# Performance work log

Hardware: AMD Instinct MI355X
Metric: run time of the kernel (lower is better)

## Reference

```python
import jax, jax.numpy as jnp
import numpy as np

B, T, D, H, O, E, K = 2, 2048, 1024, 4096, 1024, 8, 2


def setup_inputs() -> dict:
    key = jax.random.key(0)
    ks = jax.random.split(key, 10)
    s = 0.02  # small init scale to keep activations well-conditioned
    return {
        "x": jax.random.normal(ks[0], (B, T, D), jnp.float32),
        "noise": jax.random.normal(ks[1], (B, T, E), jnp.float32),
        "Wg": jax.random.normal(ks[2], (D, E), jnp.float32) * s,
        "bg": jnp.zeros((E,), jnp.float32),
        "Wn": jax.random.normal(ks[3], (D, E), jnp.float32) * s,
        "bn": jnp.zeros((E,), jnp.float32),
        "W1": jax.random.normal(ks[4], (E, D, H), jnp.float32) * s,
        "b1": jnp.zeros((E, H), jnp.float32),
        "W2": jax.random.normal(ks[5], (E, H, O), jnp.float32) * s,
        "b2": jnp.zeros((E, O), jnp.float32),
    }


def reference(x, noise, Wg, bg, Wn, bn, W1, b1, W2, b2):
    # --- NoisyTopkRouter ---
    logits = x @ Wg + bg                    # [B,T,E]
    noise_logits = x @ Wn + bn              # [B,T,E]
    noisy = logits + noise * jax.nn.softplus(noise_logits)
    top_v, top_i = jax.lax.top_k(noisy, K)  # [B,T,K]
    # scatter top-k logits into a -inf background, softmax -> sparse gates
    mask = jax.nn.one_hot(top_i, E, dtype=noisy.dtype).sum(-2)  # [B,T,E] in {0,1}
    sparse_logits = jnp.where(mask > 0, noisy, -jnp.inf)
    gating = jax.nn.softmax(sparse_logits, axis=-1)
    # mask + L1 normalize (F.normalize p=1, dim=2)
    gating = gating * mask
    gating = gating / jnp.maximum(jnp.sum(jnp.abs(gating), axis=-1, keepdims=True), 1e-12)
    # --- dense run of ALL experts (faithful to the naive torch module) ---
    h = jax.nn.relu(jnp.einsum('btd,edh->beth', x, W1) + b1[:, None, :])   # [B,E,T,H]
    expert_out = jnp.einsum('beth,eho->beto', h, W2) + b2[:, None, :]       # [B,E,T,O]
    # combine: torch transposes to [B,T,E,O] then einsum 'bte,bteo->bto'
    out = jnp.einsum('bte,beto->bto', gating, expert_out)                   # [B,T,O]
    return out
```

## Files before the change

kernel.cpp:

```cpp
#include <hip/hip_runtime.h>
#include <hip/hip_bf16.h>

#define TOK 4096
#define DD  1024
#define HH  4096
#define OO  1024
#define EE  8

#define TPE        16
#define SLOT_STRUCT (EE * TPE)
#define SLOT_OVF   64
#define SLOT_TOTAL (SLOT_STRUCT + SLOT_OVF)
#define MAX_ACTIVE 72

typedef float  f32x4  __attribute__((ext_vector_type(4)));
typedef __bf16 bf16x8 __attribute__((ext_vector_type(8)));
typedef __bf16 bf16x4 __attribute__((ext_vector_type(4)));
typedef unsigned int u32x4 __attribute__((ext_vector_type(4)));

union ABCast { u32x4 u; bf16x8 b; };

typedef __attribute__((address_space(3))) unsigned int       lds_uint;
typedef const __attribute__((address_space(1))) unsigned int glob_uint;

__device__ __forceinline__ void gload_lds16(void* lds, const void* g) {
    __builtin_amdgcn_global_load_lds((glob_uint*)g, (lds_uint*)lds, 16, 0, 0);
}

__global__ void router_kernel(const float* __restrict__ x, const float* __restrict__ noise,
                              const float* __restrict__ Wg, const float* __restrict__ bg,
                              const float* __restrict__ Wn, const float* __restrict__ bn,
                              int* __restrict__ topk_e, float* __restrict__ topk_g,
                              int* __restrict__ cnt)
{
    int wave = threadIdx.x >> 6;
    int lane = threadIdx.x & 63;
    int token = blockIdx.x * 4 + wave;
    const float* xr = x + (size_t)token * DD;
    float accg[EE], accn[EE];
#pragma unroll
    for (int e = 0; e < EE; ++e) { accg[e] = 0.f; accn[e] = 0.f; }
    for (int jj = 0; jj < DD / 64; ++jj) {
        int d = lane + jj * 64;
        float xv = xr[d];
        const float* wgr = Wg + d * EE;
        const float* wnr = Wn + d * EE;
#pragma unroll
        for (int e = 0; e < EE; ++e) {
            accg[e] += xv * wgr[e];
            accn[e] += xv * wnr[e];
        }
    }
#pragma unroll
    for (int off = 32; off; off >>= 1) {
#pragma unroll
        for (int e = 0; e < EE; ++e) {
            accg[e] += __shfl_down(accg[e], off, 64);
            accn[e] += __shfl_down(accn[e], off, 64);
        }
    }
    if (lane == 0) {
        float noisy[EE];
#pragma unroll
        for (int e = 0; e < EE; ++e) {
            float lg = accg[e] + bg[e];
            float nl = accn[e] + bn[e];
            float sp = fmaxf(nl, 0.f) + log1pf(expf(-fabsf(nl)));
            noisy[e] = lg + noise[(size_t)token * EE + e] * sp;
        }
        int i1 = 0; float v1 = noisy[0];
#pragma unroll
        for (int e = 1; e < EE; ++e) if (noisy[e] > v1) { v1 = noisy[e]; i1 = e; }
        int i2 = -1; float v2 = -1e30f;
#pragma unroll
        for (int e = 0; e < EE; ++e) if (e != i1 && noisy[e] > v2) { v2 = noisy[e]; i2 = e; }
        float ex = expf(v2 - v1);
        float g1 = 1.f / (1.f + ex);
        float g2 = ex / (1.f + ex);
        topk_e[token * 2] = i1;  topk_e[token * 2 + 1] = i2;
        topk_g[token * 2] = g1;  topk_g[token * 2 + 1] = g2;
        atomicAdd(&cnt[i1], 1);
        atomicAdd(&cnt[i2], 1);
    }
}

__global__ void plan_kernel(const int* __restrict__ cnt,
                            int* __restrict__ s_e, int* __restrict__ s_rows,
                            int* __restrict__ s_cbase, int* __restrict__ ov_base,
                            int* __restrict__ fill)
{
    if (threadIdx.x == 0 && blockIdx.x == 0) {
        for (int s = 0; s < SLOT_TOTAL; ++s) { s_e[s] = -1; s_rows[s] = 0; s_cbase[s] = 0; }
        int c = 0, ovn = 0;
        for (int e = 0; e < EE; ++e) {
            fill[e] = 0;
            ov_base[e] = ovn;
            int tiles = (cnt[e] + 127) >> 7;
            for (int t = 0; t < tiles; ++t) {
                int slot = (t < TPE) ? (e * TPE + t) : (SLOT_STRUCT + ovn + (t - TPE));
                s_e[slot] = e;
                s_rows[slot] = min(128, cnt[e] - t * 128);
                s_cbase[slot] = c * 128;
                ++c;
            }
            if (tiles > TPE) ovn += tiles - TPE;
        }
    }
}

__global__ void scatter_kernel(const int* __restrict__ topk_e, const float* __restrict__ topk_g,
                               const int* __restrict__ s_cbase, const int* __restrict__ ov_base,
                               int* __restrict__ fill,
                               int* __restrict__ row_token, float* __restrict__ row_gate)
{
    int t = blockIdx.x * blockDim.x + threadIdx.x;
    if (t >= TOK * 2) return;
    int e = topk_e[t];
    int pos = atomicAdd(&fill[e], 1);
    int tile = pos >> 7;
    int slot = (tile < TPE) ? (e * TPE + tile) : (SLOT_STRUCT + ov_base[e] + (tile - TPE));
    int crow = s_cbase[slot] + (pos & 127);
    row_token[crow] = t >> 1;
    row_gate[crow] = topk_g[t];
}

__global__ void convert_x_kernel(const float* __restrict__ in, __bf16* __restrict__ out)
{
    int i = blockIdx.x * blockDim.x + threadIdx.x;
    f32x4 v = ((const f32x4*)in)[i];
    bf16x4 o;
    o.x = (__bf16)v.x; o.y = (__bf16)v.y; o.z = (__bf16)v.z; o.w = (__bf16)v.w;
    ((bf16x4*)out)[i] = o;
}

__global__ void transpose_cvt_kernel(const float* __restrict__ in, __bf16* __restrict__ out,
                                     int R, int C)
{
    __shared__ __bf16 tile[64 * 68];
    int e = blockIdx.z;
    const float* ine = in + (size_t)e * R * C;
    __bf16* oute = out + (size_t)e * R * C;
    int c0 = blockIdx.x * 64, r0 = blockIdx.y * 64;
    int tx = threadIdx.x & 15, ty = threadIdx.x >> 4;
#pragma unroll
    for (int i = 0; i < 4; ++i) {
        int r = ty + i * 16;
        f32x4 v = *(const f32x4*)&ine[(size_t)(r0 + r) * C + c0 + tx * 4];
        tile[(4 * tx + 0) * 68 + r] = (__bf16)v.x;
        tile[(4 * tx + 1) * 68 + r] = (__bf16)v.y;
        tile[(4 * tx + 2) * 68 + r] = (__bf16)v.z;
        tile[(4 * tx + 3) * 68 + r] = (__bf16)v.w;
    }
    __syncthreads();
    int c = threadIdx.x >> 2, q = threadIdx.x & 3;
#pragma unroll
    for (int it = 0; it < 4; ++it) {
        int r4 = q * 4 + it * 16;
        bf16x4 vv = *(const bf16x4*)&tile[c * 68 + r4];
        *(bf16x4*)&oute[(size_t)(c0 + c) * R + r0 + r4] = vv;
    }
}

__global__ void gemm1_kernel(const __bf16* __restrict__ xb,
                             const __bf16* __restrict__ W1t,
                             const float* __restrict__ b1bias,
                             const int* __restrict__ s_e, const int* __restrict__ s_rows,
                             const int* __restrict__ s_cbase,
                             const int* __restrict__ row_token,
                             __bf16* __restrict__ h)
{
    int lin = blockIdx.x;
    int slot, nt;
    if (lin < EE * TPE * (HH / 128)) {
        int eb = lin & 7, r = lin >> 3;
        slot = eb * TPE + (r & 15);
        nt = r >> 4;
    } else {
        int idx = lin - EE * TPE * (HH / 128);
        nt = idx & 31;
        slot = SLOT_STRUCT + (idx >> 5);
    }
    int e = s_e[slot];
    if (e < 0) return;
    int rows_in = s_rows[slot];
    int cb = s_cbase[slot];
    int n0 = nt * 128;

    __shared__ u32x4 Alds[512];
    __shared__ u32x4 Blds[512];

    int tid = threadIdx.x;
    int wv = tid >> 6, lane = tid & 63;

    int row0 = tid >> 2;
    int kc0 = (tid & 3) ^ ((tid >> 3) & 3);
    int tok0 = (row0 < rows_in) ? row_token[cb + row0] : 0;
    int tok1 = (row0 + 64 < rows_in) ? row_token[cb + row0 + 64] : 0;
    const char* ag0 = (const char*)xb + ((size_t)tok0 * DD + kc0 * 8) * 2;
    const char* ag1 = (const char*)xb + ((size_t)tok1 * DD + kc0 * 8) * 2;
    const char* bg0 = (const char*)W1t + ((size_t)e * HH * DD + (size_t)(n0 + row0) * DD + kc0 * 8) * 2;
    const char* bg1 = bg0 + (size_t)64 * DD * 2;

    int wm = wv & 1, wn = wv >> 1;
    int quad = lane >> 4, l16 = lane & 15;
    int swz = quad ^ ((l16 >> 1) & 3);

    f32x4 acc[4][4];
#pragma unroll
    for (int i = 0; i < 4; ++i)
#pragma unroll
        for (int j = 0; j < 4; ++j) acc[i][j] = (f32x4)(0.0f);

    for (int kb = 0; kb < DD * 2; kb += 64) {
        __syncthreads();
        gload_lds16(&Alds[wv * 64],       ag0 + kb);
        gload_lds16(&Alds[256 + wv * 64], ag1 + kb);
        gload_lds16(&Blds[wv * 64],       bg0 + kb);
        gload_lds16(&Blds[256 + wv * 64], bg1 + kb);
        __syncthreads();
        ABCast af[4], bfr[4];
#pragma unroll
        for (int mf = 0; mf < 4; ++mf) af[mf].u = Alds[(wm * 64 + mf * 16 + l16) * 4 + swz];
#pragma unroll
        for (int nf = 0; nf < 4; ++nf) bfr[nf].u = Blds[(wn * 64 + nf * 16 + l16) * 4 + swz];
#pragma unroll
        for (int mf = 0; mf < 4; ++mf)
#pragma unroll
            for (int nf = 0; nf < 4; ++nf)
                acc[mf][nf] = __builtin_amdgcn_mfma_f32_16x16x32_bf16(af[mf].b, bfr[nf].b, acc[mf][nf], 0, 0, 0);
    }

#pragma unroll
    for (int mf = 0; mf < 4; ++mf) {
        int rl = wm * 64 + mf * 16 + quad * 4;
#pragma unroll
        for (int i = 0; i < 4; ++i) {
            int rli = rl + i;
            if (rli < rows_in) {
                size_t hrow = (size_t)(cb + rli) * HH;
#pragma unroll
                for (int nf = 0; nf < 4; ++nf) {
                    int col = n0 + wn * 64 + nf * 16 + l16;
                    float v = acc[mf][nf][i] + b1bias[e * HH + col];
                    v = fmaxf(v, 0.f);
                    h[hrow + col] = (__bf16)v;
                }
            }
        }
    }
}

__global__ void gemm2_kernel(const __bf16* __restrict__ h,
                             const __bf16* __restrict__ W2t,
                             const float* __restrict__ b2bias,
                             const int* __restrict__ s_e, const int* __restrict__ s_rows,
                             const int* __restrict__ s_cbase,
                             const int* __restrict__ row_token, const float* __restrict__ row_gate,
                             float* __restrict__ out)
{
    int lin = blockIdx.x;
    int slot, nt, kz;
    if (lin < EE * TPE * (OO / 128) * 2) {
        int eb = lin & 7, r = lin >> 3;
        slot = eb * TPE + (r & 15);
        int r2 = r >> 4;
        nt = r2 & 7;
        kz = r2 >> 3;
    } else {
        int idx = lin - EE * TPE * (OO / 128) * 2;
        nt = idx & 7;
        kz = (idx >> 3) & 1;
        slot = SLOT_STRUCT + (idx >> 4);
    }
    int e = s_e[slot];
    if (e < 0) return;
    int rows_in = s_rows[slot];
    int cb = s_cbase[slot];
    int n0 = nt * 128;

    __shared__ u32x4 Alds[512];
    __shared__ u32x4 Blds[512];

    int tid = threadIdx.x;
    int wv = tid >> 6, lane = tid & 63;

    int row0 = tid >> 2;
    int kc0 = (tid & 3) ^ ((tid >> 3) & 3);
    const char* ag0 = (const char*)h + ((size_t)(cb + row0) * HH + kc0 * 8) * 2;
    const char* ag1 = ag0 + (size_t)64 * HH * 2;
    const char* bg0 = (const char*)W2t + ((size_t)e * OO * HH + (size_t)(n0 + row0) * HH + kc0 * 8) * 2;
    const char* bg1 = bg0 + (size_t)64 * HH * 2;

    int wm = wv & 1, wn = wv >> 1;
    int quad = lane >> 4, l16 = lane & 15;
    int swz = quad ^ ((l16 >> 1) & 3);

    f32x4 acc[4][4];
#pragma unroll
    for (int i = 0; i < 4; ++i)
#pragma unroll
        for (int j = 0; j < 4; ++j) acc[i][j] = (f32x4)(0.0f);

    int kb0 = kz * 4096;
    for (int kb = kb0; kb < kb0 + 4096; kb += 64) {
        __syncthreads();
        gload_lds16(&Alds[wv * 64],       ag0 + kb);
        gload_lds16(&Alds[256 + wv * 64], ag1 + kb);
        gload_lds16(&Blds[wv * 64],       bg0 + kb);
        gload_lds16(&Blds[256 + wv * 64], bg1 + kb);
        __syncthreads();
        ABCast af[4], bfr[4];
#pragma unroll
        for (int mf = 0; mf < 4; ++mf) af[mf].u = Alds[(wm * 64 + mf * 16 + l16) * 4 + swz];
#pragma unroll
        for (int nf = 0; nf < 4; ++nf) bfr[nf].u = Blds[(wn * 64 + nf * 16 + l16) * 4 + swz];
#pragma unroll
        for (int mf = 0; mf < 4; ++mf)
#pragma unroll
            for (int nf = 0; nf < 4; ++nf)
                acc[mf][nf] = __builtin_amdgcn_mfma_f32_16x16x32_bf16(af[mf].b, bfr[nf].b, acc[mf][nf], 0, 0, 0);
    }

#pragma unroll
    for (int mf = 0; mf < 4; ++mf) {
        int rl = wm * 64 + mf * 16 + quad * 4;
#pragma unroll
        for (int i = 0; i < 4; ++i) {
            int rli = rl + i;
            if (rli < rows_in) {
                int token = row_token[cb + rli];
                float gate = row_gate[cb + rli];
                float* orow = out + (size_t)token * OO;
#pragma unroll
                for (int nf = 0; nf < 4; ++nf) {
                    int col = n0 + wn * 64 + nf * 16 + l16;
                    float v = acc[mf][nf][i];
                    if (kz == 0) v += b2bias[e * OO + col];
                    atomicAdd(&orow[col], gate * v);
                }
            }
        }
    }
}

extern "C" void kernel_launch(void* const* d_in, const int* in_sizes, int n_in,
                              void* d_out, int out_size, void* d_ws, size_t ws_size,
                              hipStream_t stream)
{
    const float* x     = (const float*)d_in[0];
    const float* noise = (const float*)d_in[1];
    const float* Wg    = (const float*)d_in[2];
    const float* bg    = (const float*)d_in[3];
    const float* Wn    = (const float*)d_in[4];
    const float* bn    = (const float*)d_in[5];
    const float* W1    = (const float*)d_in[6];
    const float* b1    = (const float*)d_in[7];
    const float* W2    = (const float*)d_in[8];
    const float* b2    = (const float*)d_in[9];
    float* out = (float*)d_out;

    char* p = (char*)d_ws;
    auto alloc = [&](size_t bytes) { char* r = p; p += (bytes + 255) & ~(size_t)255; return r; };
    __bf16* xb   = (__bf16*)alloc((size_t)TOK * DD * 2);
    __bf16* W1t  = (__bf16*)alloc((size_t)EE * DD * HH * 2);
    __bf16* W2t  = (__bf16*)alloc((size_t)EE * HH * OO * 2);
    __bf16* hbuf = (__bf16*)alloc((size_t)MAX_ACTIVE * 128 * HH * 2);
    int*   topk_e    = (int*)alloc((size_t)TOK * 2 * 4);
    float* topk_g    = (float*)alloc((size_t)TOK * 2 * 4);
    int*   row_token = (int*)alloc((size_t)MAX_ACTIVE * 128 * 4);
    float* row_gate  = (float*)alloc((size_t)MAX_ACTIVE * 128 * 4);
    int*   cnt       = (int*)alloc(EE * 4);
    int*   fill      = (int*)alloc(EE * 4);
    int*   ov_base   = (int*)alloc(EE * 4);
    int*   s_e       = (int*)alloc(SLOT_TOTAL * 4);
    int*   s_rows    = (int*)alloc(SLOT_TOTAL * 4);
    int*   s_cbase   = (int*)alloc(SLOT_TOTAL * 4);

    hipMemsetAsync(out, 0, (size_t)out_size * 4, stream);
    hipMemsetAsync(cnt, 0, EE * 4, stream);

    router_kernel<<<TOK / 4, 256, 0, stream>>>(x, noise, Wg, bg, Wn, bn, topk_e, topk_g, cnt);
    plan_kernel<<<1, 64, 0, stream>>>(cnt, s_e, s_rows, s_cbase, ov_base, fill);
    scatter_kernel<<<(TOK * 2) / 256, 256, 0, stream>>>(topk_e, topk_g, s_cbase, ov_base, fill,
                                                        row_token, row_gate);
    convert_x_kernel<<<(TOK * DD / 4) / 256, 256, 0, stream>>>(x, xb);
    transpose_cvt_kernel<<<dim3(HH / 64, DD / 64, EE), 256, 0, stream>>>(W1, W1t, DD, HH);
    transpose_cvt_kernel<<<dim3(OO / 64, HH / 64, EE), 256, 0, stream>>>(W2, W2t, HH, OO);

    int g1_blocks = EE * TPE * (HH / 128) + SLOT_OVF * (HH / 128);
    gemm1_kernel<<<g1_blocks, 256, 0, stream>>>(xb, W1t, b1, s_e, s_rows, s_cbase, row_token, hbuf);
    int g2_blocks = EE * TPE * (OO / 128) * 2 + SLOT_OVF * (OO / 128) * 2;
    gemm2_kernel<<<g2_blocks, 256, 0, stream>>>(hbuf, W2t, b2, s_e, s_rows, s_cbase,
                                                row_token, row_gate, out);
}
```

Measured before the change: 750.5 us.

## Double GEMM K-tile, widen LDS swizzle, split GEMM2 K four ways, shrink slot grid

```diff
diff --git a/kernel.cpp b/kernel.cpp
--- a/kernel.cpp
+++ b/kernel.cpp
@@ -7,11 +7,13 @@
 #define OO  1024
 #define EE  8
 
-#define TPE        16
+#define TPE        10
 #define SLOT_STRUCT (EE * TPE)
-#define SLOT_OVF   64
+#define SLOT_OVF   48
 #define SLOT_TOTAL (SLOT_STRUCT + SLOT_OVF)
 #define MAX_ACTIVE 72
+
+#define KSPLIT2 4
 
 typedef float  f32x4  __attribute__((ext_vector_type(4)));
 typedef __bf16 bf16x8 __attribute__((ext_vector_type(8)));
@@ -173,8 +175,8 @@
     int slot, nt;
     if (lin < EE * TPE * (HH / 128)) {
         int eb = lin & 7, r = lin >> 3;
-        slot = eb * TPE + (r & 15);
-        nt = r >> 4;
+        slot = eb * TPE + (r % TPE);
+        nt = r / TPE;
     } else {
         int idx = lin - EE * TPE * (HH / 128);
         nt = idx & 31;
@@ -186,24 +188,27 @@
     int cb = s_cbase[slot];
     int n0 = nt * 128;
 
-    __shared__ u32x4 Alds[512];
-    __shared__ u32x4 Blds[512];
+    __shared__ u32x4 Alds[1024];
+    __shared__ u32x4 Blds[1024];
 
     int tid = threadIdx.x;
     int wv = tid >> 6, lane = tid & 63;
 
-    int row0 = tid >> 2;
-    int kc0 = (tid & 3) ^ ((tid >> 3) & 3);
-    int tok0 = (row0 < rows_in) ? row_token[cb + row0] : 0;
-    int tok1 = (row0 + 64 < rows_in) ? row_token[cb + row0 + 64] : 0;
-    const char* ag0 = (const char*)xb + ((size_t)tok0 * DD + kc0 * 8) * 2;
-    const char* ag1 = (const char*)xb + ((size_t)tok1 * DD + kc0 * 8) * 2;
-    const char* bg0 = (const char*)W1t + ((size_t)e * HH * DD + (size_t)(n0 + row0) * DD + kc0 * 8) * 2;
-    const char* bg1 = bg0 + (size_t)64 * DD * 2;
+    int rbase = tid >> 3;
+    int kc = (tid & 7) ^ (rbase & 7);
+    const char* ag[4];
+    const char* bg[4];
+    const __bf16* bbase = W1t + (size_t)e * HH * DD + (size_t)n0 * DD;
+#pragma unroll
+    for (int j = 0; j < 4; ++j) {
+        int row = rbase + 32 * j;
+        int tok = (row < rows_in) ? row_token[cb + row] : 0;
+        ag[j] = (const char*)xb + ((size_t)tok * DD + kc * 8) * 2;
+        bg[j] = (const char*)(bbase + (size_t)row * DD + kc * 8);
+    }
 
     int wm = wv & 1, wn = wv >> 1;
     int quad = lane >> 4, l16 = lane & 15;
-    int swz = quad ^ ((l16 >> 1) & 3);
 
     f32x4 acc[4][4];
 #pragma unroll
@@ -211,23 +216,33 @@
 #pragma unroll
         for (int j = 0; j < 4; ++j) acc[i][j] = (f32x4)(0.0f);
 
-    for (int kb = 0; kb < DD * 2; kb += 64) {
+    for (int kb = 0; kb < DD * 2; kb += 128) {
         __syncthreads();
-        gload_lds16(&Alds[wv * 64],       ag0 + kb);
-        gload_lds16(&Alds[256 + wv * 64], ag1 + kb);
-        gload_lds16(&Blds[wv * 64],       bg0 + kb);
-        gload_lds16(&Blds[256 + wv * 64], bg1 + kb);
+#pragma unroll
+        for (int j = 0; j < 4; ++j) {
+            gload_lds16(&Alds[j * 256 + wv * 64], ag[j] + kb);
+            gload_lds16(&Blds[j * 256 + wv * 64], bg[j] + kb);
+        }
         __syncthreads();
-        ABCast af[4], bfr[4];
-#pragma unroll
-        for (int mf = 0; mf < 4; ++mf) af[mf].u = Alds[(wm * 64 + mf * 16 + l16) * 4 + swz];
-#pragma unroll
-        for (int nf = 0; nf < 4; ++nf) bfr[nf].u = Blds[(wn * 64 + nf * 16 + l16) * 4 + swz];
-#pragma unroll
-        for (int mf = 0; mf < 4; ++mf)
-#pragma unroll
-            for (int nf = 0; nf < 4; ++nf)
-                acc[mf][nf] = __builtin_amdgcn_mfma_f32_16x16x32_bf16(af[mf].b, bfr[nf].b, acc[mf][nf], 0, 0, 0);
+#pragma unroll
+        for (int s = 0; s < 2; ++s) {
+            ABCast af[4], bfr[4];
+#pragma unroll
+            for (int mf = 0; mf < 4; ++mf) {
+                int r = wm * 64 + mf * 16 + l16;
+                af[mf].u = Alds[r * 8 + ((s * 4 + quad) ^ (l16 & 7))];
+            }
+#pragma unroll
+            for (int nf = 0; nf < 4; ++nf) {
+                int r = wn * 64 + nf * 16 + l16;
+                bfr[nf].u = Blds[r * 8 + ((s * 4 + quad) ^ (l16 & 7))];
+            }
+#pragma unroll
+            for (int mf = 0; mf < 4; ++mf)
+#pragma unroll
+                for (int nf = 0; nf < 4; ++nf)
+                    acc[mf][nf] = __builtin_amdgcn_mfma_f32_16x16x32_bf16(af[mf].b, bfr[nf].b, acc[mf][nf], 0, 0, 0);
+        }
     }
 
 #pragma unroll
@@ -260,17 +275,17 @@
 {
     int lin = blockIdx.x;
     int slot, nt, kz;
-    if (lin < EE * TPE * (OO / 128) * 2) {
+    if (lin < EE * TPE * (OO / 128) * KSPLIT2) {
         int eb = lin & 7, r = lin >> 3;
-        slot = eb * TPE + (r & 15);
-        int r2 = r >> 4;
-        nt = r2 & 7;
-        kz = r2 >> 3;
+        slot = eb * TPE + (r % TPE);
+        int rest = r / TPE;
+        nt = rest & 7;
+        kz = rest >> 3;
     } else {
-        int idx = lin - EE * TPE * (OO / 128) * 2;
+        int idx = lin - EE * TPE * (OO / 128) * KSPLIT2;
         nt = idx & 7;
-        kz = (idx >> 3) & 1;
-        slot = SLOT_STRUCT + (idx >> 4);
+        kz = (idx >> 3) & 3;
+        slot = SLOT_STRUCT + (idx >> 5);
     }
     int e = s_e[slot];
     if (e < 0) return;
@@ -278,22 +293,26 @@
     int cb = s_cbase[slot];
     int n0 = nt * 128;
 
-    __shared__ u32x4 Alds[512];
-    __shared__ u32x4 Blds[512];
+    __shared__ u32x4 Alds[1024];
+    __shared__ u32x4 Blds[1024];
 
     int tid = threadIdx.x;
     int wv = tid >> 6, lane = tid & 63;
 
-    int row0 = tid >> 2;
-    int kc0 = (tid & 3) ^ ((tid >> 3) & 3);
-    const char* ag0 = (const char*)h + ((size_t)(cb + row0) * HH + kc0 * 8) * 2;
-    const char* ag1 = ag0 + (size_t)64 * HH * 2;
-    const char* bg0 = (const char*)W2t + ((size_t)e * OO * HH + (size_t)(n0 + row0) * HH + kc0 * 8) * 2;
-    const char* bg1 = bg0 + (size_t)64 * HH * 2;
+    int rbase = tid >> 3;
+    int kc = (tid & 7) ^ (rbase & 7);
+    const char* ag[4];
+    const char* bg[4];
+    const __bf16* bbase = W2t + (size_t)e * OO * HH + (size_t)n0 * HH;
+#pragma unroll
+    for (int j = 0; j < 4; ++j) {
+        int row = rbase + 32 * j;
+        ag[j] = (const char*)(h + (size_t)(cb + row) * HH + kc * 8);
+        bg[j] = (const char*)(bbase + (size_t)row * HH + kc * 8);
+    }
 
     int wm = wv & 1, wn = wv >> 1;
     int quad = lane >> 4, l16 = lane & 15;
-    int swz = quad ^ ((l16 >> 1) & 3);
 
     f32x4 acc[4][4];
 #pragma unroll
@@ -301,24 +320,34 @@
 #pragma unroll
         for (int j = 0; j < 4; ++j) acc[i][j] = (f32x4)(0.0f);
 
-    int kb0 = kz * 4096;
-    for (int kb = kb0; kb < kb0 + 4096; kb += 64) {
+    int kb0 = kz * (HH / KSPLIT2) * 2;
+    for (int kb = kb0; kb < kb0 + (HH / KSPLIT2) * 2; kb += 128) {
         __syncthreads();
-        gload_lds16(&Alds[wv * 64],       ag0 + kb);
-        gload_lds16(&Alds[256 + wv * 64], ag1 + kb);
-        gload_lds16(&Blds[wv * 64],       bg0 + kb);
-        gload_lds16(&Blds[256 + wv * 64], bg1 + kb);
+#pragma unroll
+        for (int j = 0; j < 4; ++j) {
+            gload_lds16(&Alds[j * 256 + wv * 64], ag[j] + kb);
+            gload_lds16(&Blds[j * 256 + wv * 64], bg[j] + kb);
+        }
         __syncthreads();
-        ABCast af[4], bfr[4];
-#pragma unroll
-        for (int mf = 0; mf < 4; ++mf) af[mf].u = Alds[(wm * 64 + mf * 16 + l16) * 4 + swz];
-#pragma unroll
-        for (int nf = 0; nf < 4; ++nf) bfr[nf].u = Blds[(wn * 64 + nf * 16 + l16) * 4 + swz];
-#pragma unroll
-        for (int mf = 0; mf < 4; ++mf)
-#pragma unroll
-            for (int nf = 0; nf < 4; ++nf)
-                acc[mf][nf] = __builtin_amdgcn_mfma_f32_16x16x32_bf16(af[mf].b, bfr[nf].b, acc[mf][nf], 0, 0, 0);
+#pragma unroll
+        for (int s = 0; s < 2; ++s) {
+            ABCast af[4], bfr[4];
+#pragma unroll
+            for (int mf = 0; mf < 4; ++mf) {
+                int r = wm * 64 + mf * 16 + l16;
+                af[mf].u = Alds[r * 8 + ((s * 4 + quad) ^ (l16 & 7))];
+            }
+#pragma unroll
+            for (int nf = 0; nf < 4; ++nf) {
+                int r = wn * 64 + nf * 16 + l16;
+                bfr[nf].u = Blds[r * 8 + ((s * 4 + quad) ^ (l16 & 7))];
+            }
+#pragma unroll
+            for (int mf = 0; mf < 4; ++mf)
+#pragma unroll
+                for (int nf = 0; nf < 4; ++nf)
+                    acc[mf][nf] = __builtin_amdgcn_mfma_f32_16x16x32_bf16(af[mf].b, bfr[nf].b, acc[mf][nf], 0, 0, 0);
+        }
     }
 
 #pragma unroll
@@ -389,7 +418,7 @@
 
     int g1_blocks = EE * TPE * (HH / 128) + SLOT_OVF * (HH / 128);
     gemm1_kernel<<<g1_blocks, 256, 0, stream>>>(xb, W1t, b1, s_e, s_rows, s_cbase, row_token, hbuf);
-    int g2_blocks = EE * TPE * (OO / 128) * 2 + SLOT_OVF * (OO / 128) * 2;
+    int g2_blocks = EE * TPE * (OO / 128) * KSPLIT2 + SLOT_OVF * (OO / 128) * KSPLIT2;
     gemm2_kernel<<<g2_blocks, 256, 0, stream>>>(hbuf, W2t, b2, s_e, s_rows, s_cbase,
                                                 row_token, row_gate, out);
 }
```

Result: no change. 757.3 us (+0.9%).
